# Optimization experiments

Hardware: AMD Instinct MI355X
Metric: run time of the kernel (lower is better)

## Reference

```python
import jax, jax.numpy as jnp
import numpy as np

B, N, E, H = 256, 128, 256, 512
NEG = -1e30  # stand-in for -inf in masked_fill (avoids inf-inf NaNs under vjp)


def _lstm_cell(x, h, c, Wih, Whh, bih, bhh):
    # torch LSTM gate order: i, f, g, o
    z = x @ Wih.T + h @ Whh.T + bih + bhh  # [B, 4H]
    i, f, g, o = jnp.split(z, 4, axis=-1)
    c = jax.nn.sigmoid(f) * c + jax.nn.sigmoid(i) * jnp.tanh(g)
    h = jax.nn.sigmoid(o) * jnp.tanh(c)
    return h, c


def _forward(adj_matrix, target_seq, W_embed, b_embed,
             enc_Wih, enc_Whh, enc_bih, enc_bhh,
             dec_Wih, dec_Whh, dec_bih, dec_bhh,
             decoder_start, enc_eos):
    batch, n = adj_matrix.shape[0], adj_matrix.shape[1]
    T = target_seq.shape[1]

    # input embedding: Linear(input_dim=n -> E) applied row-wise
    node_embeds = jnp.einsum('bnd,ed->bne', adj_matrix, W_embed) + b_embed  # [B,n,E]

    # ---- encoder LSTM over the n node embeddings ----
    h0 = jnp.zeros((batch, H), adj_matrix.dtype)
    c0 = jnp.zeros((batch, H), adj_matrix.dtype)

    def enc_step(carry, x_t):
        h, c = carry
        h, c = _lstm_cell(x_t, h, c, enc_Wih, enc_Whh, enc_bih, enc_bhh)
        return (h, c), h

    (enc_h, enc_c), enc_out = jax.lax.scan(enc_step, (h0, c0),
                                           node_embeds.transpose(1, 0, 2))
    enc_out = enc_out.transpose(1, 0, 2)  # [B, n, H]

    # extended encoder memory with learned EOS slot: [B, n+1, H]
    ext_enc = jnp.concatenate(
        [enc_out, jnp.broadcast_to(enc_eos, (batch, 1, H))], axis=1)

    # ---- decoder: teacher-forced pointer attention ----
    dec_input0 = jnp.broadcast_to(decoder_start, (batch, E))
    mask0 = jnp.zeros((batch, n + 1), dtype=bool)
    brange = jnp.arange(batch)

    def dec_step(carry, tgt_t):
        h, c, mask, dec_in, loss = carry
        h, c = _lstm_cell(dec_in, h, c, dec_Wih, dec_Whh, dec_bih, dec_bhh)
        logits = jnp.einsum('bnh,bh->bn', ext_enc, h)          # [B, n+1]
        logits = jnp.where(mask, NEG, logits)
        logp = jax.nn.log_softmax(logits, axis=-1)
        loss = loss - logp[brange, tgt_t].sum()                # CE, reduction='sum'
        mask = mask | jax.nn.one_hot(tgt_t, n + 1, dtype=bool)
        # next decoder input: node embedding of target, zeros if EOS (idx == n)
        emb = node_embeds[brange, jnp.clip(tgt_t, 0, n - 1)]   # [B, E]
        dec_in = jnp.where((tgt_t == n)[:, None], 0.0, emb)
        return (h, c, mask, dec_in, loss), None

    (_, _, _, _, total_loss), _ = jax.lax.scan(
        dec_step, (enc_h, enc_c, mask0, dec_input0, jnp.float32(0.0)),
        target_seq.T)
    return total_loss / (batch * T)


def setup_inputs() -> dict:
    key = jax.random.key(0)
    ks = jax.random.split(key, 16)
    u = lambda k, shape, s: jax.random.uniform(k, shape, jnp.float32, -s, s)
    kH = 1.0 / np.sqrt(H)
    adj = jax.random.normal(ks[0], (B, N, N), jnp.float32)
    adj = 0.5 * (adj + adj.transpose(0, 2, 1))  # symmetric adjacency
    # target sequences: per-row permutations of 0..N (incl. EOS token N)
    tgt = jax.vmap(lambda k: jax.random.permutation(k, N + 1))(
        jax.random.split(ks[1], B)).astype(jnp.int64)
    return {
        'adj_matrix': adj,
        'target_seq': tgt,
        'W_embed': u(ks[2], (E, N), 1.0 / np.sqrt(N)),
        'b_embed': u(ks[3], (E,), 1.0 / np.sqrt(N)),
        'enc_Wih': u(ks[4], (4 * H, E), kH),
        'enc_Whh': u(ks[5], (4 * H, H), kH),
        'enc_bih': u(ks[6], (4 * H,), kH),
        'enc_bhh': u(ks[7], (4 * H,), kH),
        'dec_Wih': u(ks[8], (4 * H, E), kH),
        'dec_Whh': u(ks[9], (4 * H, H), kH),
        'dec_bih': u(ks[10], (4 * H,), kH),
        'dec_bhh': u(ks[11], (4 * H,), kH),
        'decoder_start': u(ks[12], (E,), 0.1),
        'enc_eos': u(ks[13], (H,), 0.1),
    }


def reference(adj_matrix, target_seq, W_embed, b_embed,
              enc_Wih, enc_Whh, enc_bih, enc_bhh,
              dec_Wih, dec_Whh, dec_bih, dec_bhh,
              decoder_start, enc_eos):
    return _forward(adj_matrix, target_seq, W_embed, b_embed,
                    enc_Wih, enc_Whh, enc_bih, enc_bhh,
                    dec_Wih, dec_Whh, dec_bih, dec_bhh,
                    decoder_start, enc_eos)
```

## Files before the change

kernel.cpp:

```cpp
#include <hip/hip_runtime.h>
#include <hip/hip_bf16.h>

constexpr int B_ = 256;
constexpr int N_ = 128;
constexpr int E_ = 256;
constexpr int H_ = 512;
constexpr int T_ = 129;
constexpr float NEGV = -1e30f;

typedef __attribute__((ext_vector_type(8))) short bf16x8;
typedef __attribute__((ext_vector_type(4))) float f32x4;

__device__ __forceinline__ float sigm(float x) { return 1.0f / (1.0f + __expf(-x)); }

__device__ __forceinline__ short f2bf(float f) {
    union { float f; unsigned int u; } v; v.f = f;
    unsigned int r = (v.u + 0x7FFFu + ((v.u >> 16) & 1u)) >> 16;
    return (short)r;
}

__global__ __launch_bounds__(256)
void k_embed(const float* __restrict__ adj, const float* __restrict__ Wemb,
             const float* __restrict__ bemb, ushort* __restrict__ ne) {
    __shared__ float Wl[32][E_];
    __shared__ float As[16][33];
    const int row0 = blockIdx.x * 16;
    const int tid = threadIdx.x;
    float acc[16];
#pragma unroll
    for (int r = 0; r < 16; ++r) acc[r] = 0.f;

    for (int k0 = 0; k0 < N_; k0 += 32) {
        for (int idx = tid; idx < 32 * E_; idx += 256) {
            int kk = idx >> 8, e = idx & 255;
            Wl[kk][e] = Wemb[e * N_ + k0 + kk];
        }
        for (int idx = tid; idx < 16 * 32; idx += 256) {
            int r = idx >> 5, kk = idx & 31;
            As[r][kk] = adj[(size_t)(row0 + r) * N_ + k0 + kk];
        }
        __syncthreads();
#pragma unroll 8
        for (int kk = 0; kk < 32; ++kk) {
            float w = Wl[kk][tid];
#pragma unroll
            for (int r = 0; r < 16; ++r) acc[r] += As[r][kk] * w;
        }
        __syncthreads();
    }
    float be = bemb[tid];
#pragma unroll
    for (int r = 0; r < 16; ++r)
        ne[(size_t)(row0 + r) * E_ + tid] = (ushort)f2bf(acc[r] + be);
}

__global__ void k_init(const int* __restrict__ tgt, const float* __restrict__ eos,
                       ushort* __restrict__ hbuf0, float* __restrict__ cbuf,
                       float* __restrict__ loss, int* __restrict__ pos,
                       ushort* __restrict__ ext) {
    int idx = blockIdx.x * blockDim.x + threadIdx.x;
    if (idx < B_ * H_) { hbuf0[idx] = 0; cbuf[idx] = 0.f; }
    if (idx == 0) loss[0] = 0.f;
    if (idx < B_ * T_) {
        int b = idx / T_, t = idx % T_;
        pos[b * T_ + tgt[b * T_ + t]] = t;
    }
    if (idx < B_ * H_) {
        int b = idx / H_, u = idx % H_;
        ext[((size_t)b * T_ + N_) * H_ + u] = (ushort)f2bf(eos[u]);
    }
}

__global__ __launch_bounds__(256)
void k_decx(const int* __restrict__ tgt, const ushort* __restrict__ ne,
            const float* __restrict__ dstart, ushort* __restrict__ dx) {
    int bt = blockIdx.x;
    int b = bt / T_, t = bt % T_;
    int e = threadIdx.x;
    ushort v;
    if (t == 0) v = (ushort)f2bf(dstart[e]);
    else {
        int tg = tgt[b * T_ + t - 1];
        v = (tg >= N_) ? (ushort)0 : ne[((size_t)b * N_ + tg) * E_ + e];
    }
    dx[(size_t)bt * E_ + e] = v;
}

__global__ __launch_bounds__(256)
void k_wprep(const float* __restrict__ eWih, const float* __restrict__ eWhh,
             const float* __restrict__ dWih, const float* __restrict__ dWhh,
             ushort* __restrict__ wpack) {
    int gid = blockIdx.x * 256 + threadIdx.x;
    int lane = gid & 63;
    int rem = gid >> 6;
    int kc = rem % 24;  rem /= 24;
    int wave = rem & 3; rem >>= 2;
    int ut = rem & 31;  rem >>= 5;
    int phase = rem;
    if (phase > 1) return;

    const float* Wih = phase ? dWih : eWih;
    const float* Whh = phase ? dWhh : eWhh;
    const int l15 = lane & 15, l4 = lane >> 4;
    const int grow = wave * H_ + ut * 16 + l15;
    const float* src = (kc < 8) ? (Wih + (size_t)grow * E_ + kc * 32 + l4 * 8)
                                : (Whh + (size_t)grow * H_ + (kc - 8) * 32 + l4 * 8);
    float4 v0 = reinterpret_cast<const float4*>(src)[0];
    float4 v1 = reinterpret_cast<const float4*>(src)[1];
    ushort f[8];
    f[0] = (ushort)f2bf(v0.x); f[1] = (ushort)f2bf(v0.y);
    f[2] = (ushort)f2bf(v0.z); f[3] = (ushort)f2bf(v0.w);
    f[4] = (ushort)f2bf(v1.x); f[5] = (ushort)f2bf(v1.y);
    f[6] = (ushort)f2bf(v1.z); f[7] = (ushort)f2bf(v1.w);
    *reinterpret_cast<uint4*>(wpack + (size_t)gid * 8) = *reinterpret_cast<uint4*>(f);
}

__global__ __launch_bounds__(256)
void k_step(const ushort* __restrict__ xb, int xstr,
            const ushort* __restrict__ hc, ushort* __restrict__ hn,
            float* __restrict__ cb,
            const ushort* __restrict__ wpack_ph,
            const float* __restrict__ bih, const float* __restrict__ bhh,
            ushort* __restrict__ sv_t) {
    __shared__ ushort Alds[96 * 32 * 8];
    __shared__ float zlds[4][2][16][17];
    __shared__ float blds[64];

    const int wg = blockIdx.x;
    const int bt = wg >> 5, ut = wg & 31;
    const int b0 = bt * 32, u0 = ut * 16;
    const int tid = threadIdx.x;
    const int wave = tid >> 6;
    const int lane = tid & 63;
    const int l15 = lane & 15, l4 = lane >> 4;
    const int cj = tid & 15, cr = tid >> 4;

    bf16x8 w[24];
    const ushort* wp = wpack_ph + ((size_t)(ut * 4 + wave) * 24 * 64) * 8;
#pragma unroll
    for (int kc = 0; kc < 24; ++kc)
        w[kc] = *reinterpret_cast<const bf16x8*>(wp + ((size_t)kc * 64 + lane) * 8);

    if (tid < 64) {
        int g = tid >> 4, j = tid & 15;
        blds[tid] = bih[g * H_ + u0 + j] + bhh[g * H_ + u0 + j];
    }

#pragma unroll
    for (int i = 0; i < 12; ++i) {
        int slot = i * 256 + tid;
        int kcs = slot >> 5, row = slot & 31;
        const ushort* src = (i < 4)
            ? (xb + (size_t)(b0 + row) * xstr + kcs * 8)
            : (hc + (size_t)(b0 + row) * H_ + (kcs - 32) * 8);
        uint4 v = *reinterpret_cast<const uint4*>(src);
        *reinterpret_cast<uint4*>(&Alds[slot * 8]) = v;
    }
    __syncthreads();

    f32x4 acc0 = {0.f, 0.f, 0.f, 0.f};
    f32x4 acc1 = {0.f, 0.f, 0.f, 0.f};
#pragma unroll
    for (int kc = 0; kc < 24; ++kc) {
        const int sbase = (kc * 4 + l4) * 32;
        bf16x8 a0 = *reinterpret_cast<const bf16x8*>(&Alds[(sbase + l15) * 8]);
        bf16x8 a1 = *reinterpret_cast<const bf16x8*>(&Alds[(sbase + 16 + l15) * 8]);
        acc0 = __builtin_amdgcn_mfma_f32_16x16x32_bf16(a0, w[kc], acc0, 0, 0, 0);
        acc1 = __builtin_amdgcn_mfma_f32_16x16x32_bf16(a1, w[kc], acc1, 0, 0, 0);
    }
#pragma unroll
    for (int q = 0; q < 4; ++q) {
        zlds[wave][0][l4 * 4 + q][l15] = acc0[q];
        zlds[wave][1][l4 * 4 + q][l15] = acc1[q];
    }
    __syncthreads();

#pragma unroll
    for (int rr = 0; rr < 2; ++rr) {
        int r16 = cr + rr * 16;
        int row = b0 + r16;
        float zi = zlds[0][rr][cr][cj] + blds[cj];
        float zf = zlds[1][rr][cr][cj] + blds[16 + cj];
        float zg = zlds[2][rr][cr][cj] + blds[32 + cj];
        float zo = zlds[3][rr][cr][cj] + blds[48 + cj];
        float c_old = cb[(size_t)row * H_ + u0 + cj];
        float cn = sigm(zf) * c_old + sigm(zi) * tanhf(zg);
        float hv = sigm(zo) * tanhf(cn);
        cb[(size_t)row * H_ + u0 + cj] = cn;
        ushort hbits = (ushort)f2bf(hv);
        hn[(size_t)row * H_ + u0 + cj] = hbits;
        sv_t[(size_t)row * (T_ * H_) + u0 + cj] = hbits;
    }
}

constexpr int TT = 16;
__global__ __launch_bounds__(512)
void k_attn(const __hip_bfloat16* __restrict__ ext,
            const __hip_bfloat16* __restrict__ hdec,
            const int* __restrict__ pos, const int* __restrict__ tgt,
            float* __restrict__ loss) {
    __shared__ float ht[TT][H_];
    __shared__ float key[H_];
    __shared__ float lg[TT][T_ + 3];
    __shared__ float bl[TT];
    const int b = blockIdx.x / 9;
    const int t0 = (blockIdx.x % 9) * TT;
    const int tid = threadIdx.x;
    const int g = tid >> 5, l = tid & 31;

    for (int idx = tid; idx < TT * H_; idx += 512) {
        int tl = idx >> 9, u = idx & 511;
        int t = t0 + tl;
        ht[tl][u] = (t < T_) ? __bfloat162float(hdec[((size_t)b * T_ + t) * H_ + u]) : 0.f;
    }
    __syncthreads();

    for (int j = 0; j < T_; ++j) {
        key[tid] = __bfloat162float(ext[((size_t)b * T_ + j) * H_ + tid]);
        __syncthreads();
        float s = 0.f;
#pragma unroll
        for (int q = 0; q < H_ / 32; ++q) s += ht[g][l + q * 32] * key[l + q * 32];
        s += __shfl_xor(s, 16); s += __shfl_xor(s, 8); s += __shfl_xor(s, 4);
        s += __shfl_xor(s, 2);  s += __shfl_xor(s, 1);
        if (l == 0) {
            int t = t0 + g;
            lg[g][j] = (t < T_ && pos[b * T_ + j] < t) ? NEGV : s;
        }
        __syncthreads();
    }

    const int t = t0 + g;
    float mx = -3.4e38f;
    for (int j = l; j < T_; j += 32) mx = fmaxf(mx, lg[g][j]);
    mx = fmaxf(mx, __shfl_xor(mx, 16)); mx = fmaxf(mx, __shfl_xor(mx, 8));
    mx = fmaxf(mx, __shfl_xor(mx, 4));  mx = fmaxf(mx, __shfl_xor(mx, 2));
    mx = fmaxf(mx, __shfl_xor(mx, 1));
    float se = 0.f;
    for (int j = l; j < T_; j += 32) se += __expf(lg[g][j] - mx);
    se += __shfl_xor(se, 16); se += __shfl_xor(se, 8); se += __shfl_xor(se, 4);
    se += __shfl_xor(se, 2);  se += __shfl_xor(se, 1);
    float lval = 0.f;
    if (l == 0 && t < T_) {
        int tg = tgt[b * T_ + t];
        lval = mx + __logf(se) - lg[g][tg];
    }
    if (l == 0) bl[g] = (t < T_) ? lval : 0.f;
    __syncthreads();
    if (tid == 0) {
        float s = 0.f;
#pragma unroll
        for (int q = 0; q < TT; ++q) s += bl[q];
        atomicAdd(loss, s);
    }
}

__global__ void k_final(const float* __restrict__ loss, float* __restrict__ out) {
    out[0] = loss[0] / (float)(B_ * T_);
}

extern "C" void kernel_launch(void* const* d_in, const int* in_sizes, int n_in,
                              void* d_out, int out_size, void* d_ws, size_t ws_size,
                              hipStream_t stream) {
    const float* adj    = (const float*)d_in[0];
    const int*   tgt    = (const int*)d_in[1];
    const float* Wemb   = (const float*)d_in[2];
    const float* bemb   = (const float*)d_in[3];
    const float* eWih   = (const float*)d_in[4];
    const float* eWhh   = (const float*)d_in[5];
    const float* ebih   = (const float*)d_in[6];
    const float* ebhh   = (const float*)d_in[7];
    const float* dWih   = (const float*)d_in[8];
    const float* dWhh   = (const float*)d_in[9];
    const float* dbih   = (const float*)d_in[10];
    const float* dbhh   = (const float*)d_in[11];
    const float* dstart = (const float*)d_in[12];
    const float* eos    = (const float*)d_in[13];

    char* wsb = (char*)d_ws;
    ushort* ne    = (ushort*)wsb;  wsb += (size_t)B_ * N_ * E_ * 2;
    ushort* dxp   = (ushort*)wsb;  wsb += (size_t)B_ * T_ * E_ * 2;
    ushort* hb0   = (ushort*)wsb;  wsb += (size_t)B_ * H_ * 2;
    ushort* hb1   = (ushort*)wsb;  wsb += (size_t)B_ * H_ * 2;
    float*  cb    = (float*)wsb;   wsb += (size_t)B_ * H_ * 4;
    ushort* ext   = (ushort*)wsb;  wsb += (size_t)B_ * T_ * H_ * 2;
    ushort* hdec  = (ushort*)wsb;  wsb += (size_t)B_ * T_ * H_ * 2;
    ushort* wpack = (ushort*)wsb;  wsb += (size_t)2 * 32 * 4 * 24 * 64 * 8 * 2;
    int*    pos   = (int*)wsb;     wsb += (size_t)B_ * T_ * 4;
    float*  lacc  = (float*)wsb;

    ushort* wpackE = wpack;
    ushort* wpackD = wpack + (size_t)32 * 4 * 24 * 64 * 8;

    k_embed<<<(B_ * N_) / 16, 256, 0, stream>>>(adj, Wemb, bemb, ne);
    k_init<<<(B_ * H_) / 256, 256, 0, stream>>>(tgt, eos, hb0, cb, lacc, pos, ext);
    k_decx<<<B_ * T_, 256, 0, stream>>>(tgt, ne, dstart, dxp);
    k_wprep<<<1536, 256, 0, stream>>>(eWih, eWhh, dWih, dWhh, wpack);

    ushort* hb[2] = {hb0, hb1};

    for (int t = 0; t < N_; ++t) {
        k_step<<<256, 256, 0, stream>>>(
            ne + (size_t)t * E_, N_ * E_,
            hb[t & 1], hb[(t + 1) & 1], cb,
            wpackE, ebih, ebhh,
            ext + (size_t)t * H_);
    }
    for (int t = 0; t < T_; ++t) {
        int s = N_ + t;
        k_step<<<256, 256, 0, stream>>>(
            dxp + (size_t)t * E_, T_ * E_,
            hb[s & 1], hb[(s + 1) & 1], cb,
            wpackD, dbih, dbhh,
            hdec + (size_t)t * H_);
    }

    k_attn<<<B_ * 9, 512, 0, stream>>>((const __hip_bfloat16*)ext,
                                       (const __hip_bfloat16*)hdec, pos, tgt, lacc);
    k_final<<<1, 1, 0, stream>>>(lacc, (float*)d_out);
}
```

Baseline: 2.343 ms.

## Fuse LSTM timestep launches into one persistent cooperative kernel with flag sync

```diff
diff --git a/kernel.cpp b/kernel.cpp
--- a/kernel.cpp
+++ b/kernel.cpp
@@ -1,5 +1,6 @@
 #include <hip/hip_runtime.h>
 #include <hip/hip_bf16.h>
+#include <hip/hip_cooperative_groups.h>
 
 constexpr int B_ = 256;
 constexpr int N_ = 128;
@@ -55,12 +56,13 @@
 }
 
 __global__ void k_init(const int* __restrict__ tgt, const float* __restrict__ eos,
-                       ushort* __restrict__ hbuf0, float* __restrict__ cbuf,
-                       float* __restrict__ loss, int* __restrict__ pos,
-                       ushort* __restrict__ ext) {
+                       ushort* __restrict__ hbuf0, float* __restrict__ loss,
+                       int* __restrict__ pos, ushort* __restrict__ ext,
+                       unsigned int* __restrict__ flags) {
     int idx = blockIdx.x * blockDim.x + threadIdx.x;
-    if (idx < B_ * H_) { hbuf0[idx] = 0; cbuf[idx] = 0.f; }
+    if (idx < B_ * H_) hbuf0[idx] = 0;
     if (idx == 0) loss[0] = 0.f;
+    if (idx < 256) flags[idx] = 0;
     if (idx < B_ * T_) {
         int b = idx / T_, t = idx % T_;
         pos[b * T_ + tgt[b * T_ + t]] = t;
@@ -115,81 +117,142 @@
     *reinterpret_cast<uint4*>(wpack + (size_t)gid * 8) = *reinterpret_cast<uint4*>(f);
 }
 
-__global__ __launch_bounds__(256)
-void k_step(const ushort* __restrict__ xb, int xstr,
-            const ushort* __restrict__ hc, ushort* __restrict__ hn,
-            float* __restrict__ cb,
-            const ushort* __restrict__ wpack_ph,
-            const float* __restrict__ bih, const float* __restrict__ bhh,
-            ushort* __restrict__ sv_t) {
+__global__ __launch_bounds__(256, 1)
+void k_recur2(const ushort* __restrict__ ne, const ushort* __restrict__ dx,
+              const ushort* __restrict__ wpackE, const ushort* __restrict__ wpackD,
+              const float* __restrict__ ebih, const float* __restrict__ ebhh,
+              const float* __restrict__ dbih, const float* __restrict__ dbhh,
+              ushort* __restrict__ hb0, ushort* __restrict__ hb1,
+              ushort* __restrict__ ext, ushort* __restrict__ hdec,
+              unsigned int* __restrict__ flags) {
     __shared__ ushort Alds[96 * 32 * 8];
     __shared__ float zlds[4][2][16][17];
     __shared__ float blds[64];
 
-    const int wg = blockIdx.x;
-    const int bt = wg >> 5, ut = wg & 31;
+    const int bid = blockIdx.x;
+    const int bt = bid & 7, ut = bid >> 3;
     const int b0 = bt * 32, u0 = ut * 16;
     const int tid = threadIdx.x;
-    const int wave = tid >> 6;
-    const int lane = tid & 63;
+    const int wave = tid >> 6, lane = tid & 63;
     const int l15 = lane & 15, l4 = lane >> 4;
     const int cj = tid & 15, cr = tid >> 4;
 
+    unsigned int* flg = flags + bt * 32;
+
     bf16x8 w[24];
-    const ushort* wp = wpack_ph + ((size_t)(ut * 4 + wave) * 24 * 64) * 8;
-#pragma unroll
-    for (int kc = 0; kc < 24; ++kc)
-        w[kc] = *reinterpret_cast<const bf16x8*>(wp + ((size_t)kc * 64 + lane) * 8);
-
-    if (tid < 64) {
-        int g = tid >> 4, j = tid & 15;
-        blds[tid] = bih[g * H_ + u0 + j] + bhh[g * H_ + u0 + j];
-    }
-
-#pragma unroll
-    for (int i = 0; i < 12; ++i) {
-        int slot = i * 256 + tid;
-        int kcs = slot >> 5, row = slot & 31;
-        const ushort* src = (i < 4)
-            ? (xb + (size_t)(b0 + row) * xstr + kcs * 8)
-            : (hc + (size_t)(b0 + row) * H_ + (kcs - 32) * 8);
-        uint4 v = *reinterpret_cast<const uint4*>(src);
-        *reinterpret_cast<uint4*>(&Alds[slot * 8]) = v;
-    }
-    __syncthreads();
-
-    f32x4 acc0 = {0.f, 0.f, 0.f, 0.f};
-    f32x4 acc1 = {0.f, 0.f, 0.f, 0.f};
-#pragma unroll
-    for (int kc = 0; kc < 24; ++kc) {
-        const int sbase = (kc * 4 + l4) * 32;
-        bf16x8 a0 = *reinterpret_cast<const bf16x8*>(&Alds[(sbase + l15) * 8]);
-        bf16x8 a1 = *reinterpret_cast<const bf16x8*>(&Alds[(sbase + 16 + l15) * 8]);
-        acc0 = __builtin_amdgcn_mfma_f32_16x16x32_bf16(a0, w[kc], acc0, 0, 0, 0);
-        acc1 = __builtin_amdgcn_mfma_f32_16x16x32_bf16(a1, w[kc], acc1, 0, 0, 0);
-    }
-#pragma unroll
-    for (int q = 0; q < 4; ++q) {
-        zlds[wave][0][l4 * 4 + q][l15] = acc0[q];
-        zlds[wave][1][l4 * 4 + q][l15] = acc1[q];
-    }
-    __syncthreads();
-
-#pragma unroll
-    for (int rr = 0; rr < 2; ++rr) {
-        int r16 = cr + rr * 16;
-        int row = b0 + r16;
-        float zi = zlds[0][rr][cr][cj] + blds[cj];
-        float zf = zlds[1][rr][cr][cj] + blds[16 + cj];
-        float zg = zlds[2][rr][cr][cj] + blds[32 + cj];
-        float zo = zlds[3][rr][cr][cj] + blds[48 + cj];
-        float c_old = cb[(size_t)row * H_ + u0 + cj];
-        float cn = sigm(zf) * c_old + sigm(zi) * tanhf(zg);
-        float hv = sigm(zo) * tanhf(cn);
-        cb[(size_t)row * H_ + u0 + cj] = cn;
-        ushort hbits = (ushort)f2bf(hv);
-        hn[(size_t)row * H_ + u0 + cj] = hbits;
-        sv_t[(size_t)row * (T_ * H_) + u0 + cj] = hbits;
+    {
+        const ushort* wp = wpackE + ((size_t)(ut * 4 + wave) * 24 * 64) * 8;
+#pragma unroll
+        for (int kc = 0; kc < 24; ++kc)
+            w[kc] = *reinterpret_cast<const bf16x8*>(wp + ((size_t)kc * 64 + lane) * 8);
+        if (tid < 64)
+            blds[tid] = ebih[(tid >> 4) * H_ + u0 + (tid & 15)]
+                      + ebhh[(tid >> 4) * H_ + u0 + (tid & 15)];
+    }
+    float creg0 = 0.f, creg1 = 0.f;
+
+    for (int t = 0; t < N_ + T_; ++t) {
+        const bool enc = (t < N_);
+        const int tt = enc ? t : (t - N_);
+        const ushort* hc = (t & 1) ? hb1 : hb0;
+        ushort* hn = (t & 1) ? hb0 : hb1;
+
+        const ushort* xb = enc ? (ne + (size_t)tt * E_) : (dx + (size_t)tt * E_);
+        const int xstr = enc ? (N_ * E_) : (T_ * E_);
+#pragma unroll
+        for (int i = 0; i < 4; ++i) {
+            int slot = i * 256 + tid;
+            int kcs = slot >> 5, row = slot & 31;
+            uint4 v = *reinterpret_cast<const uint4*>(xb + (size_t)(b0 + row) * xstr + kcs * 8);
+            *reinterpret_cast<uint4*>(&Alds[slot * 8]) = v;
+        }
+
+        if (t > 0 && wave == 0) {
+            const unsigned int tv = (unsigned int)t;
+            const int fi = lane & 31;
+            while (true) {
+                unsigned int v = __hip_atomic_load(&flg[fi], __ATOMIC_RELAXED,
+                                                   __HIP_MEMORY_SCOPE_AGENT);
+                if (__all((int)(v >= tv))) break;
+                __builtin_amdgcn_s_sleep(2);
+            }
+        }
+        __syncthreads();
+
+#pragma unroll
+        for (int i = 4; i < 12; ++i) {
+            int slot = i * 256 + tid;
+            int kcs = slot >> 5, row = slot & 31;
+            const unsigned int* src = reinterpret_cast<const unsigned int*>(
+                hc + (size_t)(b0 + row) * H_ + (kcs - 32) * 8);
+            unsigned int v0 = __hip_atomic_load(&src[0], __ATOMIC_RELAXED, __HIP_MEMORY_SCOPE_AGENT);
+            unsigned int v1 = __hip_atomic_load(&src[1], __ATOMIC_RELAXED, __HIP_MEMORY_SCOPE_AGENT);
+            unsigned int v2 = __hip_atomic_load(&src[2], __ATOMIC_RELAXED, __HIP_MEMORY_SCOPE_AGENT);
+            unsigned int v3 = __hip_atomic_load(&src[3], __ATOMIC_RELAXED, __HIP_MEMORY_SCOPE_AGENT);
+            uint4 v; v.x = v0; v.y = v1; v.z = v2; v.w = v3;
+            *reinterpret_cast<uint4*>(&Alds[slot * 8]) = v;
+        }
+        __syncthreads();
+
+        f32x4 acc0 = {0.f, 0.f, 0.f, 0.f};
+        f32x4 acc1 = {0.f, 0.f, 0.f, 0.f};
+#pragma unroll
+        for (int kc = 0; kc < 24; ++kc) {
+            const int sbase = (kc * 4 + l4) * 32;
+            bf16x8 a0 = *reinterpret_cast<const bf16x8*>(&Alds[(sbase + l15) * 8]);
+            bf16x8 a1 = *reinterpret_cast<const bf16x8*>(&Alds[(sbase + 16 + l15) * 8]);
+            acc0 = __builtin_amdgcn_mfma_f32_16x16x32_bf16(a0, w[kc], acc0, 0, 0, 0);
+            acc1 = __builtin_amdgcn_mfma_f32_16x16x32_bf16(a1, w[kc], acc1, 0, 0, 0);
+        }
+#pragma unroll
+        for (int q = 0; q < 4; ++q) {
+            zlds[wave][0][l4 * 4 + q][l15] = acc0[q];
+            zlds[wave][1][l4 * 4 + q][l15] = acc1[q];
+        }
+        __syncthreads();
+
+        ushort* sv = enc ? ext : hdec;
+        ushort hbits[2];
+#pragma unroll
+        for (int rr = 0; rr < 2; ++rr) {
+            const int row = b0 + cr + rr * 16;
+            float zi = zlds[0][rr][cr][cj] + blds[cj];
+            float zf = zlds[1][rr][cr][cj] + blds[16 + cj];
+            float zg = zlds[2][rr][cr][cj] + blds[32 + cj];
+            float zo = zlds[3][rr][cr][cj] + blds[48 + cj];
+            float cold = rr ? creg1 : creg0;
+            float cn = sigm(zf) * cold + sigm(zi) * tanhf(zg);
+            float hv = sigm(zo) * tanhf(cn);
+            if (rr) creg1 = cn; else creg0 = cn;
+            hbits[rr] = (ushort)f2bf(hv);
+            sv[((size_t)row * T_ + tt) * H_ + u0 + cj] = hbits[rr];
+        }
+#pragma unroll
+        for (int rr = 0; rr < 2; ++rr) {
+            const int row = b0 + cr + rr * 16;
+            int other = __shfl_xor((int)hbits[rr], 1);
+            if ((lane & 1) == 0) {
+                unsigned int hp = ((unsigned int)hbits[rr] & 0xFFFFu)
+                                | (((unsigned int)other & 0xFFFFu) << 16);
+                unsigned int* dstp = reinterpret_cast<unsigned int*>(
+                    hn + (size_t)row * H_ + u0 + cj);
+                __hip_atomic_store(dstp, hp, __ATOMIC_RELAXED, __HIP_MEMORY_SCOPE_AGENT);
+            }
+        }
+        __syncthreads();
+        if (tid == 0)
+            __hip_atomic_store(&flg[ut], (unsigned int)(t + 1), __ATOMIC_RELAXED,
+                               __HIP_MEMORY_SCOPE_AGENT);
+
+        if (t == N_ - 1) {
+            const ushort* wp = wpackD + ((size_t)(ut * 4 + wave) * 24 * 64) * 8;
+#pragma unroll
+            for (int kc = 0; kc < 24; ++kc)
+                w[kc] = *reinterpret_cast<const bf16x8*>(wp + ((size_t)kc * 64 + lane) * 8);
+            if (tid < 64)
+                blds[tid] = dbih[(tid >> 4) * H_ + u0 + (tid & 15)]
+                          + dbhh[(tid >> 4) * H_ + u0 + (tid & 15)];
+        }
     }
 }
 
@@ -282,37 +345,35 @@
     ushort* dxp   = (ushort*)wsb;  wsb += (size_t)B_ * T_ * E_ * 2;
     ushort* hb0   = (ushort*)wsb;  wsb += (size_t)B_ * H_ * 2;
     ushort* hb1   = (ushort*)wsb;  wsb += (size_t)B_ * H_ * 2;
-    float*  cb    = (float*)wsb;   wsb += (size_t)B_ * H_ * 4;
     ushort* ext   = (ushort*)wsb;  wsb += (size_t)B_ * T_ * H_ * 2;
     ushort* hdec  = (ushort*)wsb;  wsb += (size_t)B_ * T_ * H_ * 2;
     ushort* wpack = (ushort*)wsb;  wsb += (size_t)2 * 32 * 4 * 24 * 64 * 8 * 2;
     int*    pos   = (int*)wsb;     wsb += (size_t)B_ * T_ * 4;
+    unsigned int* flags = (unsigned int*)wsb; wsb += 256 * 4;
     float*  lacc  = (float*)wsb;
 
     ushort* wpackE = wpack;
     ushort* wpackD = wpack + (size_t)32 * 4 * 24 * 64 * 8;
 
     k_embed<<<(B_ * N_) / 16, 256, 0, stream>>>(adj, Wemb, bemb, ne);
-    k_init<<<(B_ * H_) / 256, 256, 0, stream>>>(tgt, eos, hb0, cb, lacc, pos, ext);
+    k_init<<<(B_ * H_) / 256, 256, 0, stream>>>(tgt, eos, hb0, lacc, pos, ext, flags);
     k_decx<<<B_ * T_, 256, 0, stream>>>(tgt, ne, dstart, dxp);
     k_wprep<<<1536, 256, 0, stream>>>(eWih, eWhh, dWih, dWhh, wpack);
 
-    ushort* hb[2] = {hb0, hb1};
-
-    for (int t = 0; t < N_; ++t) {
-        k_step<<<256, 256, 0, stream>>>(
-            ne + (size_t)t * E_, N_ * E_,
-            hb[t & 1], hb[(t + 1) & 1], cb,
-            wpackE, ebih, ebhh,
-            ext + (size_t)t * H_);
-    }
-    for (int t = 0; t < T_; ++t) {
-        int s = N_ + t;
-        k_step<<<256, 256, 0, stream>>>(
-            dxp + (size_t)t * E_, T_ * E_,
-            hb[s & 1], hb[(s + 1) & 1], cb,
-            wpackD, dbih, dbhh,
-            hdec + (size_t)t * H_);
+    {
+        const ushort* a_ne = ne; const ushort* a_dx = dxp;
+        const ushort* a_wpE = wpackE; const ushort* a_wpD = wpackD;
+        ushort* a_hb0 = hb0; ushort* a_hb1 = hb1;
+        ushort* a_ext = ext; ushort* a_hdec = hdec;
+        unsigned int* a_flags = flags;
+        void* args[] = {
+            (void*)&a_ne, (void*)&a_dx, (void*)&a_wpE, (void*)&a_wpD,
+            (void*)&ebih, (void*)&ebhh, (void*)&dbih, (void*)&dbhh,
+            (void*)&a_hb0, (void*)&a_hb1, (void*)&a_ext, (void*)&a_hdec,
+            (void*)&a_flags
+        };
+        hipLaunchCooperativeKernel(reinterpret_cast<const void*>(&k_recur2),
+                                   dim3(256), dim3(256), args, 0, stream);
     }
 
     k_attn<<<B_ * 9, 512, 0, stream>>>((const __hip_bfloat16*)ext,
```

Measured after the change: 2.495 ms. +6.5%, slower.
